# Performance work log

Measured on AMD Instinct MI355X. Metric: run time of the kernel, lower is better.

## Reference

```python
import jax, jax.numpy as jnp
import numpy as np

N_NODES = 100000
N_EDGES = 3200000
D_IN = 512
D_HID = 512
D_OUT = 256


def setup_inputs() -> dict:
    key = jax.random.key(0)
    ks = jax.random.split(key, 7)
    x = jax.random.normal(ks[0], (N_NODES, D_IN), dtype=jnp.float32)
    edge_row = jax.random.randint(ks[1], (N_EDGES,), 0, N_NODES, dtype=jnp.int32)
    edge_col = jax.random.randint(ks[2], (N_EDGES,), 0, N_NODES, dtype=jnp.int32)
    edge_val = jax.random.uniform(ks[3], (N_EDGES,), dtype=jnp.float32)
    # Kaiming-uniform-ish init like torch Linear (bias=False)
    W0 = jax.random.normal(ks[4], (D_HID, D_IN), dtype=jnp.float32) / np.sqrt(D_IN)
    W1 = jax.random.normal(ks[5], (D_HID, D_HID), dtype=jnp.float32) / np.sqrt(D_HID)
    W2 = jax.random.normal(ks[6], (D_OUT, D_HID), dtype=jnp.float32) / np.sqrt(D_HID)
    return {"x": x, "edge_row": edge_row, "edge_col": edge_col,
            "edge_val": edge_val, "W0": W0, "W1": W1, "W2": W2}


def reference(x, edge_row, edge_col, edge_val, W0, W1, W2):
    # Layer 0: Linear (no bias) then sparse adjacency matmul (COO segment-sum)
    h = jnp.einsum('nd,hd->nh', x, W0)                      # [N, D_HID]
    msgs = edge_val[:, None] * h[edge_col]                  # gather source features [E, D_HID]
    h = jax.ops.segment_sum(msgs, edge_row, num_segments=N_NODES)  # scatter-add to rows
    h = jax.nn.relu(h)                                      # dropout p=0.0 -> identity
    # Middle layer (num_hidden=3 -> one middle layer): Linear + ReLU
    h = jax.nn.relu(jnp.einsum('nd,hd->nh', h, W1))
    # Final layer: Linear only
    out = jnp.einsum('nd,od->no', h, W2)                    # [N, D_OUT]
    return out
```

## Files before the change

### kernel.cpp

```cpp
#include <hip/hip_runtime.h>

typedef short  s16x8 __attribute__((ext_vector_type(8)));
typedef __bf16 bf16x8 __attribute__((ext_vector_type(8)));
typedef float  f32x4 __attribute__((ext_vector_type(4)));

#define AS1(p) ((const __attribute__((address_space(1))) void*)(p))
#define AS3(p) ((__attribute__((address_space(3))) void*)(p))

__device__ __forceinline__ float bf2f(short x){
  unsigned u = ((unsigned)(unsigned short)x) << 16;
  return __builtin_bit_cast(float, u);
}

__global__ void cast_f32_bf16(const float* __restrict__ in, __bf16* __restrict__ out, int n8){
  int stride = gridDim.x * blockDim.x;
  for (int i = blockIdx.x * blockDim.x + threadIdx.x; i < n8; i += stride){
    const float4* p = (const float4*)in + 2*(size_t)i;
    float4 a = p[0], b = p[1];
    bf16x8 o;
    o[0]=(__bf16)a.x; o[1]=(__bf16)a.y; o[2]=(__bf16)a.z; o[3]=(__bf16)a.w;
    o[4]=(__bf16)b.x; o[5]=(__bf16)b.y; o[6]=(__bf16)b.z; o[7]=(__bf16)b.w;
    ((bf16x8*)out)[i] = o;
  }
}

__global__ void cast3_f32_bf16(const float* __restrict__ a, __bf16* __restrict__ oa, int na8,
                               const float* __restrict__ b, __bf16* __restrict__ ob, int nb8,
                               const float* __restrict__ c, __bf16* __restrict__ oc, int nc8){
  int stride = gridDim.x * blockDim.x;
  int tot = na8 + nb8 + nc8;
  for (int i = blockIdx.x * blockDim.x + threadIdx.x; i < tot; i += stride){
    const float* in; __bf16* out; int j = i;
    if (j < na8){ in = a; out = oa; }
    else if (j < na8 + nb8){ j -= na8; in = b; out = ob; }
    else { j -= na8 + nb8; in = c; out = oc; }
    const float4* p = (const float4*)in + 2*(size_t)j;
    float4 u = p[0], v = p[1];
    bf16x8 o;
    o[0]=(__bf16)u.x; o[1]=(__bf16)u.y; o[2]=(__bf16)u.z; o[3]=(__bf16)u.w;
    o[4]=(__bf16)v.x; o[5]=(__bf16)v.y; o[6]=(__bf16)v.z; o[7]=(__bf16)v.w;
    ((bf16x8*)out)[j] = o;
  }
}

__global__ void hist_rows(const int* __restrict__ rows, int* __restrict__ counts, int n){
  int stride = gridDim.x * blockDim.x;
  for (int i = blockIdx.x * blockDim.x + threadIdx.x; i < n; i += stride)
    atomicAdd(&counts[rows[i]], 1);
}

__global__ __launch_bounds__(256) void scan_phaseA(const int* __restrict__ counts,
    int* __restrict__ rp, int* __restrict__ bsum, int n4){
  __shared__ int sb[256];
  int t = threadIdx.x;
  int idx = blockIdx.x * 256 + t;
  int4 c = make_int4(0,0,0,0);
  if (idx < n4) c = ((const int4*)counts)[idx];
  int s = c.x + c.y + c.z + c.w;
  sb[t] = s; __syncthreads();
  #pragma unroll
  for (int d = 1; d < 256; d <<= 1){
    int v = (t >= d) ? sb[t - d] : 0;
    __syncthreads();
    sb[t] += v;
    __syncthreads();
  }
  int ex = sb[t] - s;
  if (idx < n4){
    int4 o; o.x = ex; o.y = ex + c.x; o.z = o.y + c.y; o.w = o.z + c.z;
    ((int4*)rp)[idx] = o;
  }
  if (t == 255) bsum[blockIdx.x] = sb[255];
}

__global__ __launch_bounds__(128) void scan_phaseB(int* __restrict__ bsum, int nb){
  __shared__ int sb[128];
  int t = threadIdx.x;
  int v = (t < nb) ? bsum[t] : 0;
  sb[t] = v; __syncthreads();
  #pragma unroll
  for (int d = 1; d < 128; d <<= 1){
    int u = (t >= d) ? sb[t - d] : 0;
    __syncthreads();
    sb[t] += u;
    __syncthreads();
  }
  if (t < nb) bsum[t] = sb[t] - v;
}

__global__ void scan_phaseC(const int* __restrict__ bsum, int* __restrict__ rp,
    int* __restrict__ cursor, int n, int ne){
  int i = blockIdx.x * 256 + threadIdx.x;
  if (i < n){
    int v = rp[i] + bsum[i >> 10];
    rp[i] = v; cursor[i] = v;
  }
  if (i == 0) rp[n] = ne;
}

__global__ void scatter_edges(const int* __restrict__ rows, const int* __restrict__ cols,
    const float* __restrict__ vals, int* __restrict__ cursor,
    int2* __restrict__ ev, int n){
  int stride = gridDim.x * blockDim.x;
  for (int i = blockIdx.x * blockDim.x + threadIdx.x; i < n; i += stride){
    int r = rows[i];
    int p = atomicAdd(&cursor[r], 1);
    ev[p] = make_int2(cols[i], __float_as_int(vals[i]));
  }
}

__global__ __launch_bounds__(256) void spmm_relu(
    const int* __restrict__ rp, const int2* __restrict__ ev,
    const __bf16* __restrict__ H, __bf16* __restrict__ O, int n, int nwaves){
  int lane = threadIdx.x & 63;
  int w = (blockIdx.x * 256 + threadIdx.x) >> 6;
  if (w >= n) return;
  const __bf16* Hl = H + lane * 8;

  int s = rp[w], e = rp[w + 1];
  int2 cv = make_int2(0, 0);
  if (lane < e - s) cv = ev[s + lane];

  while (true){
    int wn = w + nwaves;
    int sn = 0, en = 0;
    int2 cvn = make_int2(0, 0);
    if (wn < n){
      sn = rp[wn]; en = rp[wn + 1];
      if (lane < en - sn) cvn = ev[sn + lane];
    }

    float acc[8] = {0,0,0,0,0,0,0,0};
    int deg = e - s;
    int m = deg < 64 ? deg : 64;
    int i = 0;
    for (; i + 4 <= m; i += 4){
      int c0 = __builtin_amdgcn_readlane(cv.x, i);
      int c1 = __builtin_amdgcn_readlane(cv.x, i + 1);
      int c2 = __builtin_amdgcn_readlane(cv.x, i + 2);
      int c3 = __builtin_amdgcn_readlane(cv.x, i + 3);
      float v0 = __builtin_bit_cast(float, __builtin_amdgcn_readlane(cv.y, i));
      float v1 = __builtin_bit_cast(float, __builtin_amdgcn_readlane(cv.y, i + 1));
      float v2 = __builtin_bit_cast(float, __builtin_amdgcn_readlane(cv.y, i + 2));
      float v3 = __builtin_bit_cast(float, __builtin_amdgcn_readlane(cv.y, i + 3));
      s16x8 h0 = *(const s16x8*)(Hl + (size_t)c0 * 512);
      s16x8 h1 = *(const s16x8*)(Hl + (size_t)c1 * 512);
      s16x8 h2 = *(const s16x8*)(Hl + (size_t)c2 * 512);
      s16x8 h3 = *(const s16x8*)(Hl + (size_t)c3 * 512);
      #pragma unroll
      for (int k = 0; k < 8; k++){
        acc[k] = fmaf(v0, bf2f(h0[k]), acc[k]);
        acc[k] = fmaf(v1, bf2f(h1[k]), acc[k]);
        acc[k] = fmaf(v2, bf2f(h2[k]), acc[k]);
        acc[k] = fmaf(v3, bf2f(h3[k]), acc[k]);
      }
    }
    for (; i < m; i++){
      int c = __builtin_amdgcn_readlane(cv.x, i);
      float v = __builtin_bit_cast(float, __builtin_amdgcn_readlane(cv.y, i));
      s16x8 h0 = *(const s16x8*)(Hl + (size_t)c * 512);
      #pragma unroll
      for (int k = 0; k < 8; k++) acc[k] = fmaf(v, bf2f(h0[k]), acc[k]);
    }
    for (int j = s + 64; j < e; j++){
      int2 p = ev[j];
      float v = __builtin_bit_cast(float, p.y);
      s16x8 h0 = *(const s16x8*)(Hl + (size_t)p.x * 512);
      #pragma unroll
      for (int k = 0; k < 8; k++) acc[k] = fmaf(v, bf2f(h0[k]), acc[k]);
    }

    s16x8 o;
    #pragma unroll
    for (int k = 0; k < 8; k++){
      float v = fmaxf(acc[k], 0.f);
      o[k] = __builtin_bit_cast(short, (__bf16)v);
    }
    *(s16x8*)(O + (size_t)w * 512 + lane * 8) = o;

    if (wn >= n) break;
    w = wn; s = sn; e = en; cv = cvn;
  }
}

template<int RELU, int OUT_BF16>
__global__ __launch_bounds__(256) void gemm_bt(
    const __bf16* __restrict__ A, const __bf16* __restrict__ B,
    void* __restrict__ C, int M, int N, int K){
  __shared__ __attribute__((aligned(16))) __bf16 As[128 * 64];
  __shared__ __attribute__((aligned(16))) __bf16 Bs[128 * 64];
  const int nwg = gridDim.x;
  const int q = nwg >> 3, r = nwg & 7;
  const int xcd = blockIdx.x & 7, idx = blockIdx.x >> 3;
  const int wg = (xcd < r ? xcd * (q + 1) : r * (q + 1) + (xcd - r) * q) + idx;
  const int ntiles = N >> 7;
  const int tm = wg / ntiles;
  const int tn = wg % ntiles;
  const int row0 = tm << 7, col0 = tn << 7;
  const int tid = threadIdx.x;
  const int lane = tid & 63, wid = tid >> 6;
  const int wm = (wid >> 1) * 64, wn = (wid & 1) * 64;
  const int lr = lane & 15;
  const int lkb = ((lane >> 4) * 8) * 2;

  f32x4 acc[4][4] = {};

  for (int k0 = 0; k0 < K; k0 += 64){
    __syncthreads();
    #pragma unroll
    for (int i = 0; i < 4; i++){
      int bo = tid * 16 + i * 4096;
      int rr = bo >> 7;
      int cb = bo & 127;
      int ga = row0 + rr; ga = ga < M ? ga : M - 1;
      __builtin_amdgcn_global_load_lds(AS1(A + (size_t)ga * K + k0 + (cb >> 1)),
                                       AS3((char*)As + (wid << 10) + i * 4096), 16, 0, 0);
      int gb = col0 + rr;
      __builtin_amdgcn_global_load_lds(AS1(B + (size_t)gb * K + k0 + (cb >> 1)),
                                       AS3((char*)Bs + (wid << 10) + i * 4096), 16, 0, 0);
    }
    __syncthreads();
    #pragma unroll
    for (int kk = 0; kk < 2; kk++){
      s16x8 af[4], bfr[4];
      #pragma unroll
      for (int i = 0; i < 4; i++)
        af[i] = *(const s16x8*)((const char*)As + (wm + i * 16 + lr) * 128 + kk * 64 + lkb);
      #pragma unroll
      for (int j = 0; j < 4; j++)
        bfr[j] = *(const s16x8*)((const char*)Bs + (wn + j * 16 + lr) * 128 + kk * 64 + lkb);
      #pragma unroll
      for (int i = 0; i < 4; i++)
        #pragma unroll
        for (int j = 0; j < 4; j++)
          acc[i][j] = __builtin_amdgcn_mfma_f32_16x16x32_bf16(af[i], bfr[j], acc[i][j], 0, 0, 0);
    }
  }

  const int orow = (lane >> 4) * 4;
  #pragma unroll
  for (int i = 0; i < 4; i++){
    #pragma unroll
    for (int j = 0; j < 4; j++){
      int gc = col0 + wn + j * 16 + lr;
      #pragma unroll
      for (int rr = 0; rr < 4; rr++){
        int gr = row0 + wm + i * 16 + orow + rr;
        if (gr < M){
          float v = acc[i][j][rr];
          if (RELU) v = fmaxf(v, 0.f);
          if (OUT_BF16) ((__bf16*)C)[(size_t)gr * N + gc] = (__bf16)v;
          else          ((float*)C)[(size_t)gr * N + gc] = v;
        }
      }
    }
  }
}

extern "C" void kernel_launch(void* const* d_in, const int* in_sizes, int n_in,
                              void* d_out, int out_size, void* d_ws, size_t ws_size,
                              hipStream_t stream){
  const float* x    = (const float*)d_in[0];
  const int*   erow = (const int*)d_in[1];
  const int*   ecol = (const int*)d_in[2];
  const float* eval = (const float*)d_in[3];
  const float* W0   = (const float*)d_in[4];
  const float* W1   = (const float*)d_in[5];
  const float* W2   = (const float*)d_in[6];

  const int DIN = 512, DH = 512, DO = 256;
  const int NN = in_sizes[0] / DIN;
  const int NE = in_sizes[1];

  size_t off = 0;
  auto carve = [&](size_t b) -> char* {
    char* p = (char*)d_ws + off; off += (b + 255) & ~(size_t)255; return p;
  };
  __bf16* bufA  = (__bf16*)carve((size_t)NN * DIN * 2);
  __bf16* bufB  = (__bf16*)carve((size_t)NN * DH * 2);
  __bf16* wW0   = (__bf16*)carve((size_t)DH * DIN * 2);
  __bf16* wW1   = (__bf16*)carve((size_t)DH * DH * 2);
  __bf16* wW2   = (__bf16*)carve((size_t)DO * DH * 2);
  int*   counts = (int*)carve((size_t)NN * 4);
  int*   rp     = (int*)carve(((size_t)NN + 1) * 4);
  int*   cursor = (int*)carve((size_t)NN * 4);
  int*   bsum   = (int*)carve(4096);
  int2*  ev     = (int2*)carve((size_t)NE * 8);

  hipMemsetAsync(counts, 0, (size_t)NN * 4, stream);

  cast_f32_bf16<<<4096, 256, 0, stream>>>(x, bufA, NN * DIN / 8);
  cast3_f32_bf16<<<512, 256, 0, stream>>>(W0, wW0, DH * DIN / 8,
                                          W1, wW1, DH * DH / 8,
                                          W2, wW2, DO * DH / 8);

  hist_rows<<<2048, 256, 0, stream>>>(erow, counts, NE);
  const int n4 = NN / 4;
  const int nblkA = (n4 + 255) / 256;
  scan_phaseA<<<nblkA, 256, 0, stream>>>(counts, rp, bsum, n4);
  scan_phaseB<<<1, 128, 0, stream>>>(bsum, nblkA);
  scan_phaseC<<<(NN + 255) / 256, 256, 0, stream>>>(bsum, rp, cursor, NN, NE);
  scatter_edges<<<2048, 256, 0, stream>>>(erow, ecol, eval, cursor, ev, NE);

  const int mt = (NN + 127) / 128;
  gemm_bt<0,1><<<dim3(mt * (DH / 128)), 256, 0, stream>>>(bufA, wW0, bufB, NN, DH, DIN);
  const int nwv = 2048 * 4;
  spmm_relu<<<2048, 256, 0, stream>>>(rp, ev, bufB, bufA, NN, nwv);
  gemm_bt<1,1><<<dim3(mt * (DH / 128)), 256, 0, stream>>>(bufA, wW1, bufB, NN, DH, DH);
  gemm_bt<0,0><<<dim3(mt * (DO / 128)), 256, 0, stream>>>(bufB, wW2, d_out, NN, DO, DH);
}
```

Before: 1.464 ms.

## Fuse CSR build into one cooperative kernel and merge cast launches

The separate memset, histogram, three scan phases and edge scatter kernels are replaced by a single cooperative kernel that separates the phases with grid-wide syncs. The activation cast and the three weight casts are merged into one launch. The SpMM drops its persistent, prefetching wave loop and uses one wave per row over a full-size grid. This cuts launch count and inter-kernel gaps, but it gives up the SpMM's overlap of the next row's index loads, and cooperative launch limits the grid size.

```diff
diff --git a/kernel.cpp b/kernel.cpp
--- a/kernel.cpp
+++ b/kernel.cpp
@@ -1,4 +1,7 @@
 #include <hip/hip_runtime.h>
+#include <hip/hip_cooperative_groups.h>
+
+namespace cg = cooperative_groups;
 
 typedef short  s16x8 __attribute__((ext_vector_type(8)));
 typedef __bf16 bf16x8 __attribute__((ext_vector_type(8)));
@@ -12,28 +15,18 @@
   return __builtin_bit_cast(float, u);
 }
 
-__global__ void cast_f32_bf16(const float* __restrict__ in, __bf16* __restrict__ out, int n8){
+__global__ void cast4_f32_bf16(const float* __restrict__ a, __bf16* __restrict__ oa, int na8,
+                               const float* __restrict__ b, __bf16* __restrict__ ob, int nb8,
+                               const float* __restrict__ c, __bf16* __restrict__ oc, int nc8,
+                               const float* __restrict__ d, __bf16* __restrict__ od, int nd8){
   int stride = gridDim.x * blockDim.x;
-  for (int i = blockIdx.x * blockDim.x + threadIdx.x; i < n8; i += stride){
-    const float4* p = (const float4*)in + 2*(size_t)i;
-    float4 a = p[0], b = p[1];
-    bf16x8 o;
-    o[0]=(__bf16)a.x; o[1]=(__bf16)a.y; o[2]=(__bf16)a.z; o[3]=(__bf16)a.w;
-    o[4]=(__bf16)b.x; o[5]=(__bf16)b.y; o[6]=(__bf16)b.z; o[7]=(__bf16)b.w;
-    ((bf16x8*)out)[i] = o;
-  }
-}
-
-__global__ void cast3_f32_bf16(const float* __restrict__ a, __bf16* __restrict__ oa, int na8,
-                               const float* __restrict__ b, __bf16* __restrict__ ob, int nb8,
-                               const float* __restrict__ c, __bf16* __restrict__ oc, int nc8){
-  int stride = gridDim.x * blockDim.x;
-  int tot = na8 + nb8 + nc8;
+  int tot = na8 + nb8 + nc8 + nd8;
   for (int i = blockIdx.x * blockDim.x + threadIdx.x; i < tot; i += stride){
     const float* in; __bf16* out; int j = i;
     if (j < na8){ in = a; out = oa; }
     else if (j < na8 + nb8){ j -= na8; in = b; out = ob; }
-    else { j -= na8 + nb8; in = c; out = oc; }
+    else if (j < na8 + nb8 + nc8){ j -= na8 + nb8; in = c; out = oc; }
+    else { j -= na8 + nb8 + nc8; in = d; out = od; }
     const float4* p = (const float4*)in + 2*(size_t)j;
     float4 u = p[0], v = p[1];
     bf16x8 o;
@@ -43,144 +36,133 @@
   }
 }
 
-__global__ void hist_rows(const int* __restrict__ rows, int* __restrict__ counts, int n){
-  int stride = gridDim.x * blockDim.x;
-  for (int i = blockIdx.x * blockDim.x + threadIdx.x; i < n; i += stride)
-    atomicAdd(&counts[rows[i]], 1);
-}
-
-__global__ __launch_bounds__(256) void scan_phaseA(const int* __restrict__ counts,
-    int* __restrict__ rp, int* __restrict__ bsum, int n4){
+__global__ __launch_bounds__(256) void csr_build(
+    const int* __restrict__ erow, const int* __restrict__ ecol, const float* __restrict__ eval,
+    int* __restrict__ counts, int* __restrict__ rp, int* __restrict__ cursor,
+    int* __restrict__ bsum, int2* __restrict__ ev, int NN, int NE){
+  cg::grid_group grid = cg::this_grid();
   __shared__ int sb[256];
-  int t = threadIdx.x;
-  int idx = blockIdx.x * 256 + t;
-  int4 c = make_int4(0,0,0,0);
-  if (idx < n4) c = ((const int4*)counts)[idx];
-  int s = c.x + c.y + c.z + c.w;
-  sb[t] = s; __syncthreads();
-  #pragma unroll
-  for (int d = 1; d < 256; d <<= 1){
-    int v = (t >= d) ? sb[t - d] : 0;
-    __syncthreads();
-    sb[t] += v;
-    __syncthreads();
-  }
-  int ex = sb[t] - s;
-  if (idx < n4){
-    int4 o; o.x = ex; o.y = ex + c.x; o.z = o.y + c.y; o.w = o.z + c.z;
-    ((int4*)rp)[idx] = o;
-  }
-  if (t == 255) bsum[blockIdx.x] = sb[255];
-}
-
-__global__ __launch_bounds__(128) void scan_phaseB(int* __restrict__ bsum, int nb){
-  __shared__ int sb[128];
-  int t = threadIdx.x;
-  int v = (t < nb) ? bsum[t] : 0;
-  sb[t] = v; __syncthreads();
-  #pragma unroll
-  for (int d = 1; d < 128; d <<= 1){
-    int u = (t >= d) ? sb[t - d] : 0;
-    __syncthreads();
-    sb[t] += u;
-    __syncthreads();
-  }
-  if (t < nb) bsum[t] = sb[t] - v;
-}
-
-__global__ void scan_phaseC(const int* __restrict__ bsum, int* __restrict__ rp,
-    int* __restrict__ cursor, int n, int ne){
-  int i = blockIdx.x * 256 + threadIdx.x;
-  if (i < n){
-    int v = rp[i] + bsum[i >> 10];
-    rp[i] = v; cursor[i] = v;
-  }
-  if (i == 0) rp[n] = ne;
-}
-
-__global__ void scatter_edges(const int* __restrict__ rows, const int* __restrict__ cols,
-    const float* __restrict__ vals, int* __restrict__ cursor,
-    int2* __restrict__ ev, int n){
-  int stride = gridDim.x * blockDim.x;
-  for (int i = blockIdx.x * blockDim.x + threadIdx.x; i < n; i += stride){
-    int r = rows[i];
+  __shared__ int sb2[256];
+  const int t = threadIdx.x;
+  const int gstride = gridDim.x * 256;
+  const int gtid = blockIdx.x * 256 + t;
+
+  for (int i = gtid; i < NN; i += gstride) counts[i] = 0;
+  grid.sync();
+
+  for (int i = gtid; i < NE; i += gstride) atomicAdd(&counts[erow[i]], 1);
+  grid.sync();
+
+  const int n4 = NN >> 2;
+  const int nchunk = (n4 + 255) / 256;
+  for (int chunk = blockIdx.x; chunk < nchunk; chunk += gridDim.x){
+    int idx = chunk * 256 + t;
+    int4 cc = make_int4(0,0,0,0);
+    if (idx < n4) cc = ((const int4*)counts)[idx];
+    int s = cc.x + cc.y + cc.z + cc.w;
+    sb[t] = s; __syncthreads();
+    #pragma unroll
+    for (int dd = 1; dd < 256; dd <<= 1){
+      int v = (t >= dd) ? sb[t - dd] : 0;
+      __syncthreads();
+      sb[t] += v;
+      __syncthreads();
+    }
+    int ex = sb[t] - s;
+    if (idx < n4){
+      int4 o; o.x = ex; o.y = ex + cc.x; o.z = o.y + cc.y; o.w = o.z + cc.z;
+      ((int4*)rp)[idx] = o;
+    }
+    if (t == 255) bsum[chunk] = sb[255];
+    __syncthreads();
+  }
+  grid.sync();
+
+  {
+    int v = (t < nchunk) ? bsum[t] : 0;
+    sb[t] = v; __syncthreads();
+    #pragma unroll
+    for (int dd = 1; dd < 256; dd <<= 1){
+      int u = (t >= dd) ? sb[t - dd] : 0;
+      __syncthreads();
+      sb[t] += u;
+      __syncthreads();
+    }
+    sb2[t] = sb[t] - v;
+    __syncthreads();
+    for (int i = gtid; i < NN; i += gstride){
+      int val = rp[i] + sb2[i >> 10];
+      rp[i] = val; cursor[i] = val;
+    }
+    if (gtid == 0) rp[NN] = NE;
+  }
+  grid.sync();
+
+  for (int i = gtid; i < NE; i += gstride){
+    int r = erow[i];
     int p = atomicAdd(&cursor[r], 1);
-    ev[p] = make_int2(cols[i], __float_as_int(vals[i]));
+    ev[p] = make_int2(ecol[i], __float_as_int(eval[i]));
   }
 }
 
 __global__ __launch_bounds__(256) void spmm_relu(
     const int* __restrict__ rp, const int2* __restrict__ ev,
-    const __bf16* __restrict__ H, __bf16* __restrict__ O, int n, int nwaves){
+    const __bf16* __restrict__ H, __bf16* __restrict__ O, int n){
+  int w = (blockIdx.x * 256 + threadIdx.x) >> 6;
   int lane = threadIdx.x & 63;
-  int w = (blockIdx.x * 256 + threadIdx.x) >> 6;
   if (w >= n) return;
+  int s = rp[w], e = rp[w + 1];
+  int deg = e - s;
   const __bf16* Hl = H + lane * 8;
-
-  int s = rp[w], e = rp[w + 1];
+  float acc[8] = {0,0,0,0,0,0,0,0};
+
   int2 cv = make_int2(0, 0);
-  if (lane < e - s) cv = ev[s + lane];
-
-  while (true){
-    int wn = w + nwaves;
-    int sn = 0, en = 0;
-    int2 cvn = make_int2(0, 0);
-    if (wn < n){
-      sn = rp[wn]; en = rp[wn + 1];
-      if (lane < en - sn) cvn = ev[sn + lane];
-    }
-
-    float acc[8] = {0,0,0,0,0,0,0,0};
-    int deg = e - s;
-    int m = deg < 64 ? deg : 64;
-    int i = 0;
-    for (; i + 4 <= m; i += 4){
-      int c0 = __builtin_amdgcn_readlane(cv.x, i);
-      int c1 = __builtin_amdgcn_readlane(cv.x, i + 1);
-      int c2 = __builtin_amdgcn_readlane(cv.x, i + 2);
-      int c3 = __builtin_amdgcn_readlane(cv.x, i + 3);
-      float v0 = __builtin_bit_cast(float, __builtin_amdgcn_readlane(cv.y, i));
-      float v1 = __builtin_bit_cast(float, __builtin_amdgcn_readlane(cv.y, i + 1));
-      float v2 = __builtin_bit_cast(float, __builtin_amdgcn_readlane(cv.y, i + 2));
-      float v3 = __builtin_bit_cast(float, __builtin_amdgcn_readlane(cv.y, i + 3));
-      s16x8 h0 = *(const s16x8*)(Hl + (size_t)c0 * 512);
-      s16x8 h1 = *(const s16x8*)(Hl + (size_t)c1 * 512);
-      s16x8 h2 = *(const s16x8*)(Hl + (size_t)c2 * 512);
-      s16x8 h3 = *(const s16x8*)(Hl + (size_t)c3 * 512);
-      #pragma unroll
-      for (int k = 0; k < 8; k++){
-        acc[k] = fmaf(v0, bf2f(h0[k]), acc[k]);
-        acc[k] = fmaf(v1, bf2f(h1[k]), acc[k]);
-        acc[k] = fmaf(v2, bf2f(h2[k]), acc[k]);
-        acc[k] = fmaf(v3, bf2f(h3[k]), acc[k]);
-      }
-    }
-    for (; i < m; i++){
-      int c = __builtin_amdgcn_readlane(cv.x, i);
-      float v = __builtin_bit_cast(float, __builtin_amdgcn_readlane(cv.y, i));
-      s16x8 h0 = *(const s16x8*)(Hl + (size_t)c * 512);
-      #pragma unroll
-      for (int k = 0; k < 8; k++) acc[k] = fmaf(v, bf2f(h0[k]), acc[k]);
-    }
-    for (int j = s + 64; j < e; j++){
-      int2 p = ev[j];
-      float v = __builtin_bit_cast(float, p.y);
-      s16x8 h0 = *(const s16x8*)(Hl + (size_t)p.x * 512);
-      #pragma unroll
-      for (int k = 0; k < 8; k++) acc[k] = fmaf(v, bf2f(h0[k]), acc[k]);
-    }
-
-    s16x8 o;
+  if (lane < deg) cv = ev[s + lane];
+  int m = deg < 64 ? deg : 64;
+  int i = 0;
+  for (; i + 4 <= m; i += 4){
+    int c0 = __builtin_amdgcn_readlane(cv.x, i);
+    int c1 = __builtin_amdgcn_readlane(cv.x, i + 1);
+    int c2 = __builtin_amdgcn_readlane(cv.x, i + 2);
+    int c3 = __builtin_amdgcn_readlane(cv.x, i + 3);
+    float v0 = __builtin_bit_cast(float, __builtin_amdgcn_readlane(cv.y, i));
+    float v1 = __builtin_bit_cast(float, __builtin_amdgcn_readlane(cv.y, i + 1));
+    float v2 = __builtin_bit_cast(float, __builtin_amdgcn_readlane(cv.y, i + 2));
+    float v3 = __builtin_bit_cast(float, __builtin_amdgcn_readlane(cv.y, i + 3));
+    s16x8 h0 = *(const s16x8*)(Hl + (size_t)c0 * 512);
+    s16x8 h1 = *(const s16x8*)(Hl + (size_t)c1 * 512);
+    s16x8 h2 = *(const s16x8*)(Hl + (size_t)c2 * 512);
+    s16x8 h3 = *(const s16x8*)(Hl + (size_t)c3 * 512);
     #pragma unroll
     for (int k = 0; k < 8; k++){
-      float v = fmaxf(acc[k], 0.f);
-      o[k] = __builtin_bit_cast(short, (__bf16)v);
-    }
-    *(s16x8*)(O + (size_t)w * 512 + lane * 8) = o;
-
-    if (wn >= n) break;
-    w = wn; s = sn; e = en; cv = cvn;
-  }
+      acc[k] = fmaf(v0, bf2f(h0[k]), acc[k]);
+      acc[k] = fmaf(v1, bf2f(h1[k]), acc[k]);
+      acc[k] = fmaf(v2, bf2f(h2[k]), acc[k]);
+      acc[k] = fmaf(v3, bf2f(h3[k]), acc[k]);
+    }
+  }
+  for (; i < m; i++){
+    int c = __builtin_amdgcn_readlane(cv.x, i);
+    float v = __builtin_bit_cast(float, __builtin_amdgcn_readlane(cv.y, i));
+    s16x8 h0 = *(const s16x8*)(Hl + (size_t)c * 512);
+    #pragma unroll
+    for (int k = 0; k < 8; k++) acc[k] = fmaf(v, bf2f(h0[k]), acc[k]);
+  }
+  for (int j = s + 64; j < e; j++){
+    int2 p = ev[j];
+    float v = __builtin_bit_cast(float, p.y);
+    s16x8 h0 = *(const s16x8*)(Hl + (size_t)p.x * 512);
+    #pragma unroll
+    for (int k = 0; k < 8; k++) acc[k] = fmaf(v, bf2f(h0[k]), acc[k]);
+  }
+
+  s16x8 o;
+  #pragma unroll
+  for (int k = 0; k < 8; k++){
+    float v = fmaxf(acc[k], 0.f);
+    o[k] = __builtin_bit_cast(short, (__bf16)v);
+  }
+  *(s16x8*)(O + (size_t)w * 512 + lane * 8) = o;
 }
 
 template<int RELU, int OUT_BF16>
@@ -287,25 +269,23 @@
   int*   bsum   = (int*)carve(4096);
   int2*  ev     = (int2*)carve((size_t)NE * 8);
 
-  hipMemsetAsync(counts, 0, (size_t)NN * 4, stream);
-
-  cast_f32_bf16<<<4096, 256, 0, stream>>>(x, bufA, NN * DIN / 8);
-  cast3_f32_bf16<<<512, 256, 0, stream>>>(W0, wW0, DH * DIN / 8,
-                                          W1, wW1, DH * DH / 8,
-                                          W2, wW2, DO * DH / 8);
-
-  hist_rows<<<2048, 256, 0, stream>>>(erow, counts, NE);
-  const int n4 = NN / 4;
-  const int nblkA = (n4 + 255) / 256;
-  scan_phaseA<<<nblkA, 256, 0, stream>>>(counts, rp, bsum, n4);
-  scan_phaseB<<<1, 128, 0, stream>>>(bsum, nblkA);
-  scan_phaseC<<<(NN + 255) / 256, 256, 0, stream>>>(bsum, rp, cursor, NN, NE);
-  scatter_edges<<<2048, 256, 0, stream>>>(erow, ecol, eval, cursor, ev, NE);
+  cast4_f32_bf16<<<2048, 256, 0, stream>>>(x,  bufA, NN * DIN / 8,
+                                           W0, wW0, DH * DIN / 8,
+                                           W1, wW1, DH * DH / 8,
+                                           W2, wW2, DO * DH / 8);
+
+  {
+    int nn = NN, ne = NE;
+    void* args[] = {(void*)&erow, (void*)&ecol, (void*)&eval,
+                    (void*)&counts, (void*)&rp, (void*)&cursor,
+                    (void*)&bsum, (void*)&ev, (void*)&nn, (void*)&ne};
+    hipLaunchCooperativeKernel((const void*)csr_build, dim3(1024), dim3(256),
+                               args, 0, stream);
+  }
 
   const int mt = (NN + 127) / 128;
   gemm_bt<0,1><<<dim3(mt * (DH / 128)), 256, 0, stream>>>(bufA, wW0, bufB, NN, DH, DIN);
-  const int nwv = 2048 * 4;
-  spmm_relu<<<2048, 256, 0, stream>>>(rp, ev, bufB, bufA, NN, nwv);
+  spmm_relu<<<(NN * 64 + 255) / 256, 256, 0, stream>>>(rp, ev, bufB, bufA, NN);
   gemm_bt<1,1><<<dim3(mt * (DH / 128)), 256, 0, stream>>>(bufA, wW1, bufB, NN, DH, DH);
   gemm_bt<0,0><<<dim3(mt * (DO / 128)), 256, 0, stream>>>(bufB, wW2, d_out, NN, DO, DH);
 }
```

After: 1.813 ms. +23.8%, slower.
